# Kernel optimization log

Measured on AMD Instinct MI355X. Metric: run time of the kernel, lower is better.

## Reference

```python
import jax, jax.numpy as jnp
import numpy as np

EMBED = 512
NHEAD = 16
HDIM = EMBED // NHEAD
HIDDEN = 512  # Mlp hidden is hard-coded to 512
EPS_LN = 1e-6
EPS_ATT = 1e-6


def layernorm(x, gamma, beta):
    mu = jnp.mean(x, axis=-1, keepdims=True)
    var = jnp.mean(jnp.square(x - mu), axis=-1, keepdims=True)
    return (x - mu) * jax.lax.rsqrt(var + EPS_LN) * gamma + beta


def setup_inputs() -> dict:
    key = jax.random.key(0)
    ks = jax.random.split(key, 16)
    B, N, C = 8, 4096, EMBED
    s = 1.0 / np.sqrt(C)
    inp = {
        "x": jax.random.normal(ks[0], (B, N, C), dtype=jnp.float32),
        # projection weights stored as (in, out); torch Linear uses x @ W.T
        "Wq": jax.random.normal(ks[1], (C, C), dtype=jnp.float32) * s,
        "Wk": jax.random.normal(ks[2], (C, C), dtype=jnp.float32) * s,
        "Wv": jax.random.normal(ks[3], (C, C), dtype=jnp.float32) * s,
        "Wm": jax.random.normal(ks[4], (C, C), dtype=jnp.float32) * s,
        "W1": jax.random.normal(ks[5], (C, HIDDEN), dtype=jnp.float32) * s,
        "b1": jax.random.normal(ks[6], (HIDDEN,), dtype=jnp.float32) * 1e-6,
        "W2": jax.random.normal(ks[7], (HIDDEN, C), dtype=jnp.float32) * (1.0 / np.sqrt(HIDDEN)),
        "b2": jax.random.normal(ks[8], (C,), dtype=jnp.float32) * 1e-6,
        "g_att": jnp.ones((C,), dtype=jnp.float32),
        "b_att": jnp.zeros((C,), dtype=jnp.float32),
        "g_ffn": jnp.ones((C,), dtype=jnp.float32),
        "b_ffn": jnp.zeros((C,), dtype=jnp.float32),
    }
    return inp


def reference(x, Wq, Wk, Wv, Wm, W1, b1, W2, b2, g_att, b_att, g_ffn, b_ffn):
    B, N, C = x.shape
    # --- attention sub-block ---
    h = layernorm(x, g_att, b_att)
    q = (h @ Wq).reshape(B, N, NHEAD, HDIM)
    k = (h @ Wk).reshape(B, N, NHEAD, HDIM)
    v = (h @ Wv).reshape(B, N, NHEAD, HDIM)
    Q = jax.nn.elu(q) + 1.0  # feature map: elu(x)+1
    K = jax.nn.elu(k) + 1.0
    v = v / N
    KV = jnp.einsum('nshd,nshv->nhdv', K, v)
    Z = 1.0 / (jnp.einsum('nlhd,nhd->nlh', Q, K.sum(axis=1)) + EPS_ATT)
    msg = jnp.einsum('nlhd,nhdv->nlhv', Q, KV) * Z[..., None] * N
    msg = msg.reshape(B, N, C) @ Wm
    x = x + msg
    # --- feed-forward sub-block ---
    h2 = layernorm(x, g_ffn, b_ffn)
    f = jax.nn.gelu(h2 @ W1 + b1, approximate=False) @ W2 + b2
    return x + f
```

## Files before the change

### kernel.cpp

```cpp
#include <hip/hip_runtime.h>
#include <hip/hip_bf16.h>
#include <math.h>

typedef unsigned short u16;
typedef __attribute__((ext_vector_type(8))) __bf16 bf16x8;
typedef __attribute__((ext_vector_type(4))) float floatx4;

#define SEQ   4096
#define BATCH 8
#define ROWS  32768
#define C     512
#define NH    16
#define HD    32

__device__ inline u16 f2bf(float f) {
    union { float f; unsigned u; } v; v.f = f;
    unsigned r = (v.u + 0x7FFFu + ((v.u >> 16) & 1u)) >> 16;
    return (u16)r;
}
__device__ inline float bf2f(u16 h) {
    union { unsigned u; float f; } v; v.u = ((unsigned)h) << 16;
    return v.f;
}

__device__ inline void g2lds16(const u16* g, u16* l) {
    __builtin_amdgcn_global_load_lds((const __attribute__((address_space(1))) unsigned*)g,
                                     (__attribute__((address_space(3))) unsigned*)l, 16, 0, 0);
}

__global__ __launch_bounds__(256) void prep_weights(
    const float* __restrict__ Wq, const float* __restrict__ Wk,
    const float* __restrict__ Wv, const float* __restrict__ Wm,
    const float* __restrict__ W1, const float* __restrict__ W2,
    u16* __restrict__ Wqkvt, u16* __restrict__ Wmt,
    u16* __restrict__ W1t, u16* __restrict__ W2t)
{
    int blk = blockIdx.x;
    int mat = blk >> 6;
    int tile = blk & 63;
    int k0 = (tile >> 3) * 64, n0 = (tile & 7) * 64;
    const float* src; u16* dst;
    switch (mat) {
        case 0: src = Wq; dst = Wqkvt;              break;
        case 1: src = Wk; dst = Wqkvt + 512*512;    break;
        case 2: src = Wv; dst = Wqkvt + 2*512*512;  break;
        case 3: src = Wm; dst = Wmt;                break;
        case 4: src = W1; dst = W1t;                break;
        default: src = W2; dst = W2t;               break;
    }
    __shared__ float ts[64][65];
    int t = threadIdx.x;
    #pragma unroll
    for (int i = 0; i < 16; i++) {
        int e = i * 256 + t;
        int kr = e >> 6, nc = e & 63;
        ts[kr][nc] = src[(size_t)(k0 + kr) * 512 + n0 + nc];
    }
    __syncthreads();
    #pragma unroll
    for (int i = 0; i < 2; i++) {
        int e = i * 256 + t;
        int nr = e >> 3, kc0 = (e & 7) * 8;
        union { uint4 v; u16 u[8]; } o;
        #pragma unroll
        for (int q = 0; q < 8; q++) o.u[q] = f2bf(ts[kc0 + q][nr]);
        *(uint4*)(dst + (size_t)(n0 + nr) * 512 + k0 + kc0) = o.v;
    }
}

__global__ __launch_bounds__(256) void ln_kernel(
    const float* __restrict__ in, const float* __restrict__ g,
    const float* __restrict__ b, u16* __restrict__ out)
{
    int row  = blockIdx.x * 4 + (threadIdx.x >> 6);
    int lane = threadIdx.x & 63;
    const float* p = in + (size_t)row * C + lane * 8;
    float4 v0 = *(const float4*)p;
    float4 v1 = *(const float4*)(p + 4);
    float s  = v0.x + v0.y + v0.z + v0.w + v1.x + v1.y + v1.z + v1.w;
    float s2 = v0.x*v0.x + v0.y*v0.y + v0.z*v0.z + v0.w*v0.w
             + v1.x*v1.x + v1.y*v1.y + v1.z*v1.z + v1.w*v1.w;
    #pragma unroll
    for (int off = 1; off < 64; off <<= 1) {
        s  += __shfl_xor(s, off);
        s2 += __shfl_xor(s2, off);
    }
    float mean = s * (1.f / C);
    float var  = s2 * (1.f / C) - mean * mean;
    float inv  = rsqrtf(var + 1e-6f);
    int c = lane * 8;
    float4 g0 = *(const float4*)(g + c), g1 = *(const float4*)(g + c + 4);
    float4 b0 = *(const float4*)(b + c), b1 = *(const float4*)(b + c + 4);
    union { uint4 v; u16 u[8]; } o;
    o.u[0] = f2bf((v0.x - mean) * inv * g0.x + b0.x);
    o.u[1] = f2bf((v0.y - mean) * inv * g0.y + b0.y);
    o.u[2] = f2bf((v0.z - mean) * inv * g0.z + b0.z);
    o.u[3] = f2bf((v0.w - mean) * inv * g0.w + b0.w);
    o.u[4] = f2bf((v1.x - mean) * inv * g1.x + b1.x);
    o.u[5] = f2bf((v1.y - mean) * inv * g1.y + b1.y);
    o.u[6] = f2bf((v1.z - mean) * inv * g1.z + b1.z);
    o.u[7] = f2bf((v1.w - mean) * inv * g1.w + b1.w);
    *(uint4*)(out + (size_t)row * C + c) = o.v;
}

template <int EPI>
__global__ __launch_bounds__(256, 2) void gemm_tile(
    const u16* __restrict__ A, const u16* __restrict__ Bt,
    int K, int ldc,
    u16* __restrict__ outb, float* __restrict__ outf,
    const float* __restrict__ bias, const float* __restrict__ resid)
{
    __shared__ u16 lsA[128 * 32];
    __shared__ u16 lsB[128 * 32];
    const int t = threadIdx.x;
    const int w = t >> 6, l = t & 63, lr = l & 15, quad = l >> 4;
    const int m0 = blockIdx.y * 128, n0 = blockIdx.x * 128;
    const int RW = (w >> 1) * 64, CW = (w & 1) * 64;

    floatx4 acc[4][4];
    #pragma unroll
    for (int i = 0; i < 4; i++)
        #pragma unroll
        for (int j = 0; j < 4; j++) { floatx4 z = {0.f, 0.f, 0.f, 0.f}; acc[i][j] = z; }

    const int e0 = w * 1024 + l * 8;
    const int e1 = e0 + 512;
    const u16* Ag0 = A  + (size_t)(m0 + (e0 >> 5)) * K + (e0 & 31);
    const u16* Ag1 = A  + (size_t)(m0 + (e1 >> 5)) * K + (e1 & 31);
    const u16* Bg0 = Bt + (size_t)(n0 + (e0 >> 5)) * K + (e0 & 31);
    const u16* Bg1 = Bt + (size_t)(n0 + (e1 >> 5)) * K + (e1 & 31);
    u16* lA0 = lsA + w * 1024;
    u16* lA1 = lsA + w * 1024 + 512;
    u16* lB0 = lsB + w * 1024;
    u16* lB1 = lsB + w * 1024 + 512;

    for (int kk = 0; kk < K; kk += 32) {
        __syncthreads();
        g2lds16(Ag0 + kk, lA0);
        g2lds16(Ag1 + kk, lA1);
        g2lds16(Bg0 + kk, lB0);
        g2lds16(Bg1 + kk, lB1);
        __syncthreads();
        bf16x8 af[4], bfr[4];
        #pragma unroll
        for (int i = 0; i < 4; i++) {
            af[i]  = *(const bf16x8*)(lsA + (RW + i * 16 + lr) * 32 + quad * 8);
            bfr[i] = *(const bf16x8*)(lsB + (CW + i * 16 + lr) * 32 + quad * 8);
        }
        #pragma unroll
        for (int i = 0; i < 4; i++)
            #pragma unroll
            for (int j = 0; j < 4; j++)
                acc[i][j] = __builtin_amdgcn_mfma_f32_16x16x32_bf16(af[i], bfr[j], acc[i][j], 0, 0, 0);
    }

    #pragma unroll
    for (int i = 0; i < 4; i++) {
        #pragma unroll
        for (int j = 0; j < 4; j++) {
            #pragma unroll
            for (int r = 0; r < 4; r++) {
                int row = m0 + RW + i * 16 + quad * 4 + r;
                int col = n0 + CW + j * 16 + lr;
                float v = acc[i][j][r];
                size_t idx = (size_t)row * ldc + col;
                if constexpr (EPI == 0) {
                    if (col < 1024) v = v > 0.f ? v + 1.f : __expf(v);
                    else            v *= (1.0f / SEQ);
                    outb[idx] = f2bf(v);
                } else if constexpr (EPI == 1) {
                    outf[idx] = resid[idx] + v;
                } else if constexpr (EPI == 2) {
                    v += bias[col];
                    v = 0.5f * v * (1.f + erff(v * 0.70710678118f));
                    outb[idx] = f2bf(v);
                } else {
                    outf[idx] = outf[idx] + v + bias[col];
                }
            }
        }
    }
}

__global__ __launch_bounds__(256) void zero_kernel(float* p, int n) {
    int i = blockIdx.x * 256 + threadIdx.x;
    if (i < n) p[i] = 0.f;
}

__global__ __launch_bounds__(256) void kv_reduce(
    const u16* __restrict__ qkv, float* __restrict__ KV, float* __restrict__ Ksum)
{
    int bh = blockIdx.x;
    int b = bh >> 4, h = bh & 15;
    int chunk = blockIdx.y;
    int t = threadIdx.x;
    __shared__ float Ks[32 * 32];
    __shared__ float Vs[32 * 32];
    int d  = t & 31;
    int vd = (t >> 5) << 2;
    float a0 = 0.f, a1 = 0.f, a2 = 0.f, a3 = 0.f, ks = 0.f;
    const size_t base = (size_t)b * SEQ * 1536 + 512 + h * HD;
    int j   = t & 127;
    int isV = t >> 7;
    int sl  = j >> 2, cc = (j & 3) * 8;
    float* dst = (isV ? Vs : Ks) + sl * 32 + cc;
    for (int so = 0; so < 512; so += 32) {
        size_t gp = base + (size_t)(chunk * 512 + so + sl) * 1536 + cc + (isV ? 512 : 0);
        union { uint4 v; u16 u[8]; } uu;
        uu.v = *(const uint4*)(qkv + gp);
        float f[8];
        #pragma unroll
        for (int q = 0; q < 8; q++) f[q] = bf2f(uu.u[q]);
        __syncthreads();
        *(float4*)dst       = float4{f[0], f[1], f[2], f[3]};
        *(float4*)(dst + 4) = float4{f[4], f[5], f[6], f[7]};
        __syncthreads();
        #pragma unroll
        for (int s = 0; s < 32; s++) {
            float kvv = Ks[s * 32 + d];
            float4 vv = *(const float4*)(Vs + s * 32 + vd);
            a0 += kvv * vv.x; a1 += kvv * vv.y; a2 += kvv * vv.z; a3 += kvv * vv.w;
            ks += kvv;
        }
    }
    float* kvp = KV + (size_t)bh * 1024 + d * 32 + vd;
    atomicAdd(kvp + 0, a0);
    atomicAdd(kvp + 1, a1);
    atomicAdd(kvp + 2, a2);
    atomicAdd(kvp + 3, a3);
    if (t < 32) atomicAdd(Ksum + bh * 32 + t, ks);
}

__global__ __launch_bounds__(256) void msg_kernel(
    const u16* __restrict__ qkv, const float* __restrict__ KV,
    const float* __restrict__ Ksum, u16* __restrict__ msg)
{
    int blk = blockIdx.x;
    int b = blk >> 5;
    int r0 = (blk & 31) * 128;
    int t = threadIdx.x;
    int h = t >> 4;
    int vd = (t & 15) * 2;
    float kv0[32], kv1[32], ksr[32];
    const float* kvh = KV + ((size_t)b * 16 + h) * 1024;
    const float* ksh = Ksum + (b * 16 + h) * 32;
    #pragma unroll
    for (int d = 0; d < 32; d++) {
        kv0[d] = kvh[d * 32 + vd];
        kv1[d] = kvh[d * 32 + vd + 1];
        ksr[d] = ksh[d];
    }
    __shared__ u16 Qs[4 * 512];
    const int srr = t >> 6;
    const int scc = (t & 63) * 8;
    for (int rg = 0; rg < 128; rg += 4) {
        size_t row = (size_t)b * SEQ + r0 + rg;
        uint4 qv = *(const uint4*)(qkv + (row + srr) * 1536 + scc);
        __syncthreads();
        *(uint4*)(Qs + srr * 512 + scc) = qv;
        __syncthreads();
        #pragma unroll
        for (int r2 = 0; r2 < 4; r2++) {
            const u16* qp = Qs + r2 * 512 + h * HD;
            float q[32];
            #pragma unroll
            for (int i0 = 0; i0 < 32; i0 += 8) {
                union { uint4 v; u16 u[8]; } uu;
                uu.v = *(const uint4*)(qp + i0);
                #pragma unroll
                for (int jq = 0; jq < 8; jq++) q[i0 + jq] = bf2f(uu.u[jq]);
            }
            float zdot = 0.f, m0 = 0.f, m1 = 0.f;
            #pragma unroll
            for (int d = 0; d < 32; d++) {
                float qd = q[d];
                zdot += qd * ksr[d];
                m0   += qd * kv0[d];
                m1   += qd * kv1[d];
            }
            float z = (float)SEQ / (zdot + 1e-6f);
            unsigned pack = (unsigned)f2bf(m0 * z) | ((unsigned)f2bf(m1 * z) << 16);
            *(unsigned*)(msg + (row + r2) * C + h * HD + vd) = pack;
        }
    }
}

extern "C" void kernel_launch(void* const* d_in, const int* in_sizes, int n_in,
                              void* d_out, int out_size, void* d_ws, size_t ws_size,
                              hipStream_t stream) {
    const float* x     = (const float*)d_in[0];
    const float* Wq    = (const float*)d_in[1];
    const float* Wk    = (const float*)d_in[2];
    const float* Wv    = (const float*)d_in[3];
    const float* Wm    = (const float*)d_in[4];
    const float* W1    = (const float*)d_in[5];
    const float* b1    = (const float*)d_in[6];
    const float* W2    = (const float*)d_in[7];
    const float* b2    = (const float*)d_in[8];
    const float* g_att = (const float*)d_in[9];
    const float* b_att = (const float*)d_in[10];
    const float* g_ffn = (const float*)d_in[11];
    const float* b_ffn = (const float*)d_in[12];
    float* out = (float*)d_out;

    char* ws = (char*)d_ws;
    u16*   Wqkvt = (u16*)(ws);
    u16*   Wmt   = (u16*)(ws + 0x180000);
    u16*   W1t   = (u16*)(ws + 0x200000);
    u16*   W2t   = (u16*)(ws + 0x280000);
    float* KV    = (float*)(ws + 0x300000);
    float* Ksum  = (float*)(ws + 0x380000);
    u16*   hb    = (u16*)(ws + 0x400000);
    u16*   qkv   = (u16*)(ws + 0x2400000);
    u16*   h2    = qkv;
    u16*   f1    = (u16*)(ws + 0x4400000);

    prep_weights<<<6 * 64, 256, 0, stream>>>(Wq, Wk, Wv, Wm, W1, W2,
                                             Wqkvt, Wmt, W1t, W2t);
    ln_kernel<<<ROWS / 4, 256, 0, stream>>>(x, g_att, b_att, hb);
    gemm_tile<0><<<dim3(12, 256), 256, 0, stream>>>(hb, Wqkvt, 512, 1536,
                                                    qkv, nullptr, nullptr, nullptr);
    zero_kernel<<<(128 * 1024 + 128 * 32 + 255) / 256, 256, 0, stream>>>(KV, 128 * 1024 + 128 * 32);
    kv_reduce<<<dim3(128, 8), 256, 0, stream>>>(qkv, KV, Ksum);
    msg_kernel<<<256, 256, 0, stream>>>(qkv, KV, Ksum, hb);
    gemm_tile<1><<<dim3(4, 256), 256, 0, stream>>>(hb, Wmt, 512, 512,
                                                   nullptr, out, nullptr, x);
    ln_kernel<<<ROWS / 4, 256, 0, stream>>>(out, g_ffn, b_ffn, h2);
    gemm_tile<2><<<dim3(4, 256), 256, 0, stream>>>(h2, W1t, 512, 512,
                                                   f1, nullptr, b1, nullptr);
    gemm_tile<3><<<dim3(4, 256), 256, 0, stream>>>(f1, W2t, 512, 512,
                                                   nullptr, out, b2, nullptr);
}
```

Before: 471.8 us.

## Widen GEMM K-tile to 64 with swizzled LDS and split attention reductions finer

The GEMM now stages 64-wide K slices per barrier pair instead of 32, halving the number of synchronisations. It uses an XOR-like rotation swizzle on the LDS column to avoid bank conflicts when reading fragments. Separately, kv_reduce is split into 16 sequence chunks instead of 8, and msg_kernel into 1024 blocks of 32 rows instead of 256 blocks of 128, for more parallelism. The zero kernel is replaced with hipMemsetAsync. LDS per block doubles to 32KB, which may affect occupancy, and finer kv_reduce chunks double the atomic traffic.

```diff
diff --git a/kernel.cpp b/kernel.cpp
--- a/kernel.cpp
+++ b/kernel.cpp
@@ -110,8 +110,8 @@
     u16* __restrict__ outb, float* __restrict__ outf,
     const float* __restrict__ bias, const float* __restrict__ resid)
 {
-    __shared__ u16 lsA[128 * 32];
-    __shared__ u16 lsB[128 * 32];
+    __shared__ u16 lsA[128 * 64];
+    __shared__ u16 lsB[128 * 64];
     const int t = threadIdx.x;
     const int w = t >> 6, l = t & 63, lr = l & 15, quad = l >> 4;
     const int m0 = blockIdx.y * 128, n0 = blockIdx.x * 128;
@@ -123,35 +123,36 @@
         #pragma unroll
         for (int j = 0; j < 4; j++) { floatx4 z = {0.f, 0.f, 0.f, 0.f}; acc[i][j] = z; }
 
-    const int e0 = w * 1024 + l * 8;
-    const int e1 = e0 + 512;
-    const u16* Ag0 = A  + (size_t)(m0 + (e0 >> 5)) * K + (e0 & 31);
-    const u16* Ag1 = A  + (size_t)(m0 + (e1 >> 5)) * K + (e1 & 31);
-    const u16* Bg0 = Bt + (size_t)(n0 + (e0 >> 5)) * K + (e0 & 31);
-    const u16* Bg1 = Bt + (size_t)(n0 + (e1 >> 5)) * K + (e1 & 31);
-    u16* lA0 = lsA + w * 1024;
-    u16* lA1 = lsA + w * 1024 + 512;
-    u16* lB0 = lsB + w * 1024;
-    u16* lB1 = lsB + w * 1024 + 512;
-
-    for (int kk = 0; kk < K; kk += 32) {
-        __syncthreads();
-        g2lds16(Ag0 + kk, lA0);
-        g2lds16(Ag1 + kk, lA1);
-        g2lds16(Bg0 + kk, lB0);
-        g2lds16(Bg1 + kk, lB1);
-        __syncthreads();
-        bf16x8 af[4], bfr[4];
-        #pragma unroll
-        for (int i = 0; i < 4; i++) {
-            af[i]  = *(const bf16x8*)(lsA + (RW + i * 16 + lr) * 32 + quad * 8);
-            bfr[i] = *(const bf16x8*)(lsB + (CW + i * 16 + lr) * 32 + quad * 8);
-        }
-        #pragma unroll
-        for (int i = 0; i < 4; i++)
-            #pragma unroll
-            for (int j = 0; j < 4; j++)
-                acc[i][j] = __builtin_amdgcn_mfma_f32_16x16x32_bf16(af[i], bfr[j], acc[i][j], 0, 0, 0);
+    const int srow = w * 32 + (l >> 3);
+    const int scol = (((l & 7) - (l >> 3)) & 7) * 8;
+    const u16* Ag = A  + (size_t)(m0 + srow) * K + scol;
+    const u16* Bg = Bt + (size_t)(n0 + srow) * K + scol;
+    u16* lAw = lsA + w * 2048;
+    u16* lBw = lsB + w * 2048;
+
+    for (int kk = 0; kk < K; kk += 64) {
+        __syncthreads();
+        #pragma unroll
+        for (int c = 0; c < 4; c++) {
+            g2lds16(Ag + (size_t)(c * 8) * K + kk, lAw + c * 512);
+            g2lds16(Bg + (size_t)(c * 8) * K + kk, lBw + c * 512);
+        }
+        __syncthreads();
+        #pragma unroll
+        for (int ks = 0; ks < 2; ks++) {
+            bf16x8 af[4], bfr[4];
+            const int m = ((ks * 4 + quad + (lr & 7)) & 7) * 8;
+            #pragma unroll
+            for (int i = 0; i < 4; i++) {
+                af[i]  = *(const bf16x8*)(lsA + (RW + i * 16 + lr) * 64 + m);
+                bfr[i] = *(const bf16x8*)(lsB + (CW + i * 16 + lr) * 64 + m);
+            }
+            #pragma unroll
+            for (int i = 0; i < 4; i++)
+                #pragma unroll
+                for (int j = 0; j < 4; j++)
+                    acc[i][j] = __builtin_amdgcn_mfma_f32_16x16x32_bf16(af[i], bfr[j], acc[i][j], 0, 0, 0);
+        }
     }
 
     #pragma unroll
@@ -182,11 +183,6 @@
     }
 }
 
-__global__ __launch_bounds__(256) void zero_kernel(float* p, int n) {
-    int i = blockIdx.x * 256 + threadIdx.x;
-    if (i < n) p[i] = 0.f;
-}
-
 __global__ __launch_bounds__(256) void kv_reduce(
     const u16* __restrict__ qkv, float* __restrict__ KV, float* __restrict__ Ksum)
 {
@@ -204,8 +200,8 @@
     int isV = t >> 7;
     int sl  = j >> 2, cc = (j & 3) * 8;
     float* dst = (isV ? Vs : Ks) + sl * 32 + cc;
-    for (int so = 0; so < 512; so += 32) {
-        size_t gp = base + (size_t)(chunk * 512 + so + sl) * 1536 + cc + (isV ? 512 : 0);
+    for (int so = 0; so < 256; so += 32) {
+        size_t gp = base + (size_t)(chunk * 256 + so + sl) * 1536 + cc + (isV ? 512 : 0);
         union { uint4 v; u16 u[8]; } uu;
         uu.v = *(const uint4*)(qkv + gp);
         float f[8];
@@ -236,8 +232,8 @@
     const float* __restrict__ Ksum, u16* __restrict__ msg)
 {
     int blk = blockIdx.x;
-    int b = blk >> 5;
-    int r0 = (blk & 31) * 128;
+    int b = blk >> 7;
+    int r0 = (blk & 127) * 32;
     int t = threadIdx.x;
     int h = t >> 4;
     int vd = (t & 15) * 2;
@@ -253,7 +249,7 @@
     __shared__ u16 Qs[4 * 512];
     const int srr = t >> 6;
     const int scc = (t & 63) * 8;
-    for (int rg = 0; rg < 128; rg += 4) {
+    for (int rg = 0; rg < 32; rg += 4) {
         size_t row = (size_t)b * SEQ + r0 + rg;
         uint4 qv = *(const uint4*)(qkv + (row + srr) * 1536 + scc);
         __syncthreads();
@@ -320,9 +316,9 @@
     ln_kernel<<<ROWS / 4, 256, 0, stream>>>(x, g_att, b_att, hb);
     gemm_tile<0><<<dim3(12, 256), 256, 0, stream>>>(hb, Wqkvt, 512, 1536,
                                                     qkv, nullptr, nullptr, nullptr);
-    zero_kernel<<<(128 * 1024 + 128 * 32 + 255) / 256, 256, 0, stream>>>(KV, 128 * 1024 + 128 * 32);
-    kv_reduce<<<dim3(128, 8), 256, 0, stream>>>(qkv, KV, Ksum);
-    msg_kernel<<<256, 256, 0, stream>>>(qkv, KV, Ksum, hb);
+    hipMemsetAsync(KV, 0, (128 * 1024 + 128 * 32) * sizeof(float), stream);
+    kv_reduce<<<dim3(128, 16), 256, 0, stream>>>(qkv, KV, Ksum);
+    msg_kernel<<<1024, 256, 0, stream>>>(qkv, KV, Ksum, hb);
     gemm_tile<1><<<dim3(4, 256), 256, 0, stream>>>(hb, Wmt, 512, 512,
                                                    nullptr, out, nullptr, x);
     ln_kernel<<<ROWS / 4, 256, 0, stream>>>(out, g_ffn, b_ffn, h2);
```

New measurement: 445.3 us. -5.6%, faster.
